# Kernel optimization log

Hardware: AMD Instinct MI355X
Metric: run time of the kernel (lower is better)

## Reference

```python
import jax, jax.numpy as jnp
import numpy as np

EMBED_DIM = 768
NUM_HEADS = 12
HEAD_DIM = EMBED_DIM // NUM_HEADS


def setup_inputs() -> dict:
    key = jax.random.key(0)
    ks = jax.random.split(key, 5)
    B, N, D = 8, 1024, EMBED_DIM
    s = 1.0 / np.sqrt(D)
    x = jax.random.normal(ks[0], (B, N, D), dtype=jnp.float32)
    W_qkv = jax.random.normal(ks[1], (D, 3 * D), dtype=jnp.float32) * s
    b_qkv = jnp.zeros((3 * D,), dtype=jnp.float32)
    W_proj = jax.random.normal(ks[2], (D, D), dtype=jnp.float32) * s
    b_proj = jnp.zeros((D,), dtype=jnp.float32)
    return {"x": x, "W_qkv": W_qkv, "b_qkv": b_qkv, "W_proj": W_proj, "b_proj": b_proj}


def reference(x, W_qkv, b_qkv, W_proj, b_proj):
    B, N, D = x.shape
    H, Hd = NUM_HEADS, HEAD_DIM
    scale = Hd ** -0.5
    qkv = x @ W_qkv + b_qkv                      # (B, N, 3D)
    qkv = qkv.reshape(B, N, 3, H, Hd).transpose(2, 0, 3, 1, 4)  # (3, B, H, N, Hd)
    q, k, v = qkv[0], qkv[1], qkv[2]
    attn = jnp.einsum('bhnd,bhmd->bhnm', q, k) * scale  # (B, H, N, N)
    attn = jax.nn.softmax(attn, axis=-1)
    out = jnp.einsum('bhnm,bhmd->bhnd', attn, v)        # (B, H, N, Hd)
    out = out.transpose(0, 2, 1, 3).reshape(B, N, D)
    return out @ W_proj + b_proj
```

## Files before the change

kernel.cpp:

```cpp
#include <hip/hip_runtime.h>


#define B_   8
#define N_   1024
#define D_   768
#define H_   12
#define HD_  64

typedef __attribute__((ext_vector_type(4))) float f32x4;
typedef __attribute__((ext_vector_type(8))) short bf16x8;

__device__ __forceinline__ unsigned short f2bf(float f) {
    unsigned int u = __float_as_uint(f);
    u += 0x7fff + ((u >> 16) & 1);
    return (unsigned short)(u >> 16);
}
__device__ __forceinline__ unsigned int pk2(float a, float b) {
    return (unsigned int)f2bf(a) | ((unsigned int)f2bf(b) << 16);
}
__device__ __forceinline__ unsigned int pk2t(float a, float b) {
    return __builtin_amdgcn_perm(__float_as_uint(b), __float_as_uint(a), 0x07060302u);
}
__device__ __forceinline__ float truncbf(float f) {
    return __uint_as_float(__float_as_uint(f) & 0xFFFF0000u);
}
__device__ __forceinline__ void gl_lds16(const void* g, void* l) {
    __builtin_amdgcn_global_load_lds(
        (const __attribute__((address_space(1))) unsigned int*)g,
        (__attribute__((address_space(3))) unsigned int*)l, 16, 0, 0);
}
#define MFMA(a, b, c) __builtin_amdgcn_mfma_f32_16x16x32_bf16(a, b, c, 0, 0, 0)
#define BAR() do { __asm__ volatile("" ::: "memory"); \
    __builtin_amdgcn_s_barrier(); \
    __asm__ volatile("" ::: "memory"); } while (0)
#define WAITVM(n) do { __asm__ volatile("" ::: "memory"); \
    __builtin_amdgcn_s_waitcnt(0xF70 | (n)); \
    __asm__ volatile("" ::: "memory"); } while (0)

__global__ __launch_bounds__(256) void prep_kernel(
    const float* __restrict__ x, const float* __restrict__ wqkv,
    const float* __restrict__ wproj,
    unsigned short* __restrict__ XB, unsigned short* __restrict__ WQT,
    unsigned short* __restrict__ WPT)
{
    const int bid = blockIdx.x;
    const int tid = threadIdx.x;
    if (bid < 3072) {
        int id = bid * 256 + tid;
        int r  = id & 127;
        int kc = (id >> 7) & 7;
        int ks = (id >> 10) % 12;
        int nt = id / 12288;
        const float* src = x + (size_t)(nt * 128 + r) * 768 + ks * 64 + kc * 8;
        float4 f0 = *(const float4*)src;
        float4 f1 = *(const float4*)(src + 4);
        uint4 o;
        o.x = pk2(f0.x, f0.y); o.y = pk2(f0.z, f0.w);
        o.z = pk2(f1.x, f1.y); o.w = pk2(f1.z, f1.w);
        *(uint4*)&XB[(size_t)id * 8] = o;
    } else if (bid < 3936) {
        int id = (bid - 3072) * 256 + tid;
        int fr = id & 127;
        int kc = (id >> 7) & 7;
        int ks = (id >> 10) % 12;
        int mt = id / 12288;
        float v[8];
#pragma unroll
        for (int j = 0; j < 8; ++j)
            v[j] = wqkv[(size_t)(ks * 64 + kc * 8 + j) * 2304 + mt * 128 + fr];
        uint4 o;
        o.x = pk2(v[0], v[1]); o.y = pk2(v[2], v[3]);
        o.z = pk2(v[4], v[5]); o.w = pk2(v[6], v[7]);
        *(uint4*)&WQT[(size_t)id * 8] = o;
    } else {
        int id = (bid - 3936) * 256 + tid;
        int fr = id & 63;
        int kc = (id >> 6) & 7;
        int ks = (id >> 9) % 12;
        int nt = id / 6144;
        float v[8];
#pragma unroll
        for (int j = 0; j < 8; ++j)
            v[j] = wproj[(size_t)(ks * 64 + kc * 8 + j) * 768 + nt * 64 + fr];
        uint4 o;
        o.x = pk2(v[0], v[1]); o.y = pk2(v[2], v[3]);
        o.z = pk2(v[4], v[5]); o.w = pk2(v[6], v[7]);
        *(uint4*)&WPT[(size_t)id * 8] = o;
    }
}

__global__ __launch_bounds__(256, 4) void qkv_gemm(
    const unsigned short* __restrict__ XB,
    const unsigned short* __restrict__ WQT,
    const float* __restrict__ bias,
    unsigned short* __restrict__ QS,
    unsigned short* __restrict__ KS,
    unsigned short* __restrict__ VS)
{
    __shared__ __align__(16) unsigned short As[2][4096];
    __shared__ __align__(16) unsigned short Bs[2][4096];

    const int tid = threadIdx.x;
    const int w = tid >> 6, lane = tid & 63;
    const int l15 = lane & 15, quad = lane >> 4;
    const int mt = blockIdx.x >> 6;
    const int nt = blockIdx.x & 63;
    const int m0w = (w & 1) * 64, n0w = (w >> 1) * 64;

    const char* baseA = (const char*)(WQT + (size_t)(mt * 12) * 8192);
    const char* baseB = (const char*)(XB  + (size_t)(nt * 12) * 8192);

    auto issue = [&](int ks) {
        const char* sA = baseA + ks * 8192;
        const char* sB = baseB + ks * 8192;
        const int pb = ks & 1;
#pragma unroll
        for (int i = 0; i < 2; ++i) {
            const int c = w * 2 + i;
            gl_lds16(sA + (c * 64 + lane) * 16, (char*)As + pb * 8192 + c * 1024);
            gl_lds16(sB + (c * 64 + lane) * 16, (char*)Bs + pb * 8192 + c * 1024);
        }
    };

    f32x4 acc[4][4];
    const f32x4 z = {0.f, 0.f, 0.f, 0.f};
#pragma unroll
    for (int t = 0; t < 4; ++t)
#pragma unroll
        for (int u = 0; u < 4; ++u) acc[t][u] = z;

    issue(0);
    for (int ks = 0; ks < 24; ++ks) {
        BAR();
        if (ks < 23) { issue(ks + 1); WAITVM(4); } else { WAITVM(0); }
        BAR();
        const unsigned short* Ab = As[ks & 1];
        const unsigned short* Bb = Bs[ks & 1];
        bf16x8 af[4], bfv[4];
#pragma unroll
        for (int t = 0; t < 4; ++t)
            af[t] = *(const bf16x8*)(Ab + (quad * 128 + m0w + t * 16 + l15) * 8);
#pragma unroll
        for (int u = 0; u < 4; ++u)
            bfv[u] = *(const bf16x8*)(Bb + (quad * 128 + n0w + u * 16 + l15) * 8);
#pragma unroll
        for (int t = 0; t < 4; ++t)
#pragma unroll
            for (int u = 0; u < 4; ++u)
                acc[t][u] = MFMA(af[t], bfv[u], acc[t][u]);
    }

    const int part = mt / 6;
#pragma unroll
    for (int t = 0; t < 4; ++t) {
        int flocal = (mt % 6) * 128 + m0w + t * 16 + quad * 4;
        float4 bv = *(const float4*)&bias[part * 768 + flocal];
        int h = flocal >> 6, d0 = flocal & 63;
#pragma unroll
        for (int u = 0; u < 4; ++u) {
            int token = nt * 128 + n0w + u * 16 + l15;
            int b = token >> 10, n = token & 1023;
            int bh = b * H_ + h;
            f32x4 a = acc[t][u];
            float v0 = a[0] + bv.x, v1 = a[1] + bv.y;
            float v2 = a[2] + bv.z, v3 = a[3] + bv.w;
            if (part == 0) {
                int qt = n >> 7, r = n & 127;
                size_t idx = ((size_t)(bh * 8 + qt) * 1024 + (d0 >> 3) * 128 + r) * 8 + (d0 & 7);
                uint2 pp; pp.x = pk2(v0, v1); pp.y = pk2(v2, v3);
                *(uint2*)&QS[idx] = pp;
            } else if (part == 1) {
                int kt = n >> 6, r = n & 63;
                size_t idx = ((size_t)(bh * 16 + kt) * 512 + (d0 >> 3) * 64 + r) * 8 + (d0 & 7);
                uint2 pp; pp.x = pk2(v0, v1); pp.y = pk2(v2, v3);
                *(uint2*)&KS[idx] = pp;
            } else {
                int kt = n >> 6, r = n & 63;
                size_t base = ((size_t)(bh * 16 + kt) * 512 + (r >> 3) * 64 + d0) * 8 + (r & 7);
                VS[base]      = f2bf(v0);
                VS[base + 8]  = f2bf(v1);
                VS[base + 16] = f2bf(v2);
                VS[base + 24] = f2bf(v3);
            }
        }
    }
}

__global__ __launch_bounds__(256, 3) void attn_kernel(
    const unsigned short* __restrict__ QS,
    const unsigned short* __restrict__ KS,
    const unsigned short* __restrict__ VS,
    unsigned short* __restrict__ AWS)
{
    __shared__ __align__(16) unsigned short Qs[8192];
    __shared__ __align__(16) unsigned short Ks[2][4096];
    __shared__ __align__(16) unsigned short Vs[2][4096];

    const int tid = threadIdx.x;
    const int w = tid >> 6, lane = tid & 63;
    const int l15 = lane & 15, quad = lane >> 4;
    const int bh = blockIdx.x % 96;
    const int qt = blockIdx.x / 96;
    const float C = 0.18033688f;

    const char* kbase = (const char*)(KS + (size_t)(bh * 16) * 4096);
    const char* vbase = (const char*)(VS + (size_t)(bh * 16) * 4096);

    auto issue_tile = [&](int kt) {
        const char* ks_ = kbase + kt * 8192;
        const char* vs_ = vbase + kt * 8192;
        const int pb = kt & 1;
#pragma unroll
        for (int i = 0; i < 2; ++i) {
            const int c = w * 2 + i;
            gl_lds16(ks_ + (c * 64 + lane) * 16, (char*)Ks + pb * 8192 + c * 1024);
            gl_lds16(vs_ + (c * 64 + lane) * 16, (char*)Vs + pb * 8192 + c * 1024);
        }
    };

    const char* qslab = (const char*)(QS + (size_t)(bh * 8 + qt) * 8192);
#pragma unroll
    for (int i = 0; i < 4; ++i) {
        const int c = w * 4 + i;
        gl_lds16(qslab + (c * 64 + lane) * 16, (char*)Qs + c * 1024);
    }
    issue_tile(0);

    WAITVM(4);
    BAR();
    bf16x8 qf[2][2];
#pragma unroll
    for (int u = 0; u < 2; ++u)
#pragma unroll
        for (int s = 0; s < 2; ++s)
            qf[u][s] = *(const bf16x8*)(Qs + ((s * 4 + quad) * 128 + w * 32 + u * 16 + l15) * 8);

    f32x4 o[4][2];
    const f32x4 z = {0.f, 0.f, 0.f, 0.f};
#pragma unroll
    for (int t = 0; t < 4; ++t) { o[t][0] = z; o[t][1] = z; }
    float lsum[2] = {0.f, 0.f};

    for (int kt = 0; kt < 16; ++kt) {
        BAR();
        if (kt < 15) { issue_tile(kt + 1); WAITVM(4); } else { WAITVM(0); }
        BAR();
        const unsigned short* Kb = Ks[kt & 1];
        const unsigned short* Vb = Vs[kt & 1];

        f32x4 s[4][2];
#pragma unroll
        for (int t = 0; t < 4; ++t) { s[t][0] = z; s[t][1] = z; }
#pragma unroll
        for (int ss = 0; ss < 2; ++ss) {
            bf16x8 kf[4];
#pragma unroll
            for (int t = 0; t < 4; ++t)
                kf[t] = *(const bf16x8*)(Kb + ((ss * 4 + quad) * 64 + t * 16 + l15) * 8);
#pragma unroll
            for (int t = 0; t < 4; ++t)
#pragma unroll
                for (int u = 0; u < 2; ++u)
                    s[t][u] = MFMA(kf[t], qf[u][ss], s[t][u]);
        }

        unsigned int pkk[2][4][2];
#pragma unroll
        for (int u = 0; u < 2; ++u) {
#pragma unroll
            for (int t = 0; t < 4; ++t) {
                float p0 = truncbf(__builtin_amdgcn_exp2f(s[t][u][0] * C));
                float p1 = truncbf(__builtin_amdgcn_exp2f(s[t][u][1] * C));
                float p2 = truncbf(__builtin_amdgcn_exp2f(s[t][u][2] * C));
                float p3 = truncbf(__builtin_amdgcn_exp2f(s[t][u][3] * C));
                lsum[u] += (p0 + p1) + (p2 + p3);
                pkk[u][t][0] = pk2t(p0, p1);
                pkk[u][t][1] = pk2t(p2, p3);
            }
        }

#pragma unroll
        for (int ss = 0; ss < 2; ++ss) {
            unsigned int bfr[2][4];
#pragma unroll
            for (int u = 0; u < 2; ++u)
#pragma unroll
                for (int jj = 0; jj < 4; ++jj) {
                    int sq = (quad & 1) * 2 + (jj >> 1);
                    int src = l15 + sq * 16;
                    int v0 = __shfl((int)pkk[u][2 * ss][jj & 1], src, 64);
                    int v1 = __shfl((int)pkk[u][2 * ss + 1][jj & 1], src, 64);
                    bfr[u][jj] = (quad >> 1) ? (unsigned int)v1 : (unsigned int)v0;
                }
            bf16x8 vf[4];
#pragma unroll
            for (int t = 0; t < 4; ++t)
                vf[t] = *(const bf16x8*)(Vb + ((ss * 4 + quad) * 64 + t * 16 + l15) * 8);
#pragma unroll
            for (int u = 0; u < 2; ++u) {
                union { unsigned int uu[4]; bf16x8 v; } cv;
                cv.uu[0] = bfr[u][0]; cv.uu[1] = bfr[u][1];
                cv.uu[2] = bfr[u][2]; cv.uu[3] = bfr[u][3];
#pragma unroll
                for (int t = 0; t < 4; ++t)
                    o[t][u] = MFMA(vf[t], cv.v, o[t][u]);
            }
        }
    }

    float inv[2];
#pragma unroll
    for (int u = 0; u < 2; ++u) {
        float l = lsum[u];
        l += __shfl_xor(l, 16, 64);
        l += __shfl_xor(l, 32, 64);
        inv[u] = 1.f / l;
    }
    const int b = bh / H_, h = bh % H_;
    const int mt = b * 8 + qt;
#pragma unroll
    for (int t = 0; t < 4; ++t) {
        int d0 = t * 16 + quad * 4;
#pragma unroll
        for (int u = 0; u < 2; ++u) {
            int ql = w * 32 + u * 16 + l15;
            size_t idx = ((size_t)(mt * 12 + h) * 1024 + (d0 >> 3) * 128 + ql) * 8 + (d0 & 7);
            uint2 pp;
            pp.x = pk2(o[t][u][0] * inv[u], o[t][u][1] * inv[u]);
            pp.y = pk2(o[t][u][2] * inv[u], o[t][u][3] * inv[u]);
            *(uint2*)&AWS[idx] = pp;
        }
    }
}

__global__ __launch_bounds__(256, 3) void proj_gemm(
    const unsigned short* __restrict__ AWS,
    const unsigned short* __restrict__ WPT,
    const float* __restrict__ bias, float* __restrict__ out)
{
    __shared__ __align__(16) unsigned short As[2][8192];
    __shared__ __align__(16) unsigned short Bs[2][4096];

    const int tid = threadIdx.x;
    const int w = tid >> 6, lane = tid & 63;
    const int l15 = lane & 15, quad = lane >> 4;
    const int mt = blockIdx.x / 12;
    const int nt = blockIdx.x % 12;
    const int m0w = (w & 1) * 64, n0w = (w >> 1) * 32;

    const char* baseA = (const char*)(AWS + (size_t)(mt * 12) * 8192);
    const char* baseB = (const char*)(WPT + (size_t)(nt * 12) * 4096);

    auto issue = [&](int ks) {
        const char* sA = baseA + ks * 16384;
        const char* sB = baseB + ks * 8192;
        const int pb = ks & 1;
#pragma unroll
        for (int i = 0; i < 4; ++i) {
            const int c = w * 4 + i;
            gl_lds16(sA + (c * 64 + lane) * 16, (char*)As + pb * 16384 + c * 1024);
        }
#pragma unroll
        for (int i = 0; i < 2; ++i) {
            const int c = w * 2 + i;
            gl_lds16(sB + (c * 64 + lane) * 16, (char*)Bs + pb * 8192 + c * 1024);
        }
    };

    f32x4 acc[4][2];
    const f32x4 z = {0.f, 0.f, 0.f, 0.f};
#pragma unroll
    for (int t = 0; t < 4; ++t) { acc[t][0] = z; acc[t][1] = z; }

    issue(0);
    for (int ks = 0; ks < 12; ++ks) {
        BAR();
        if (ks < 11) { issue(ks + 1); WAITVM(6); } else { WAITVM(0); }
        BAR();
        const unsigned short* Ab = As[ks & 1];
        const unsigned short* Bb = Bs[ks & 1];
#pragma unroll
        for (int kk = 0; kk < 2; ++kk) {
            bf16x8 af[4], bfv[2];
#pragma unroll
            for (int t = 0; t < 4; ++t)
                af[t] = *(const bf16x8*)(Ab + (((kk * 4 + quad) * 128) + m0w + t * 16 + l15) * 8);
#pragma unroll
            for (int u = 0; u < 2; ++u)
                bfv[u] = *(const bf16x8*)(Bb + (((kk * 4 + quad) * 64) + n0w + u * 16 + l15) * 8);
#pragma unroll
            for (int t = 0; t < 4; ++t)
#pragma unroll
                for (int u = 0; u < 2; ++u)
                    acc[t][u] = MFMA(af[t], bfv[u], acc[t][u]);
        }
    }

#pragma unroll
    for (int t = 0; t < 4; ++t)
#pragma unroll
        for (int u = 0; u < 2; ++u) {
            int col = nt * 64 + n0w + u * 16 + l15;
            float bvv = bias[col];
#pragma unroll
            for (int r = 0; r < 4; ++r) {
                int row = mt * 128 + m0w + t * 16 + quad * 4 + r;
                out[(size_t)row * 768 + col] = acc[t][u][r] + bvv;
            }
        }
}

extern "C" void kernel_launch(void* const* d_in, const int* in_sizes, int n_in,
                              void* d_out, int out_size, void* d_ws, size_t ws_size,
                              hipStream_t stream) {
    const float* x     = (const float*)d_in[0];
    const float* Wqkv  = (const float*)d_in[1];
    const float* bqkv  = (const float*)d_in[2];
    const float* Wproj = (const float*)d_in[3];
    const float* bproj = (const float*)d_in[4];
    float* out = (float*)d_out;

    unsigned short* ws = (unsigned short*)d_ws;
    unsigned short* XB  = ws;
    unsigned short* WQT = ws + 6291456;
    unsigned short* WPT = ws + 8060928;
    unsigned short* QS  = ws + 8650752;
    unsigned short* KS  = ws + 14942208;
    unsigned short* VS  = ws + 21233664;
    unsigned short* AWS = ws + 27525120;

    prep_kernel<<<dim3(4224), dim3(256), 0, stream>>>(x, Wqkv, Wproj, XB, WQT, WPT);
    qkv_gemm<<<dim3(18 * 64), dim3(256), 0, stream>>>(XB, WQT, bqkv, QS, KS, VS);
    attn_kernel<<<dim3(96 * 8), dim3(256), 0, stream>>>(QS, KS, VS, AWS);
    proj_gemm<<<dim3(64 * 12), dim3(256), 0, stream>>>(AWS, WPT, bproj, out);
}
```

Baseline: 194.2 us.

## Stage GEMM/attention epilogues through LDS and move P relayout from shuffles to LDS

The QKV GEMM epilogue now writes results into a swizzled LDS tile and then stores full 16-byte vectors to the Q/K/V tiled layouts, instead of scattered 8-byte and 2-byte global stores. The softmax scale is folded into Q at the GEMM epilogue, which removes a multiply per score in attention. In attention, the P-fragment relayout that used many cross-lane shuffles now goes through a per-wave swizzled LDS scratch area, and the output epilogue is also staged through LDS for coalesced 16-byte stores. The cost is extra barriers and LDS traffic, and the Q tile region is reused as scratch after Q fragments are loaded into registers.

```diff
diff --git a/kernel.cpp b/kernel.cpp
--- a/kernel.cpp
+++ b/kernel.cpp
@@ -36,6 +36,7 @@
 #define WAITVM(n) do { __asm__ volatile("" ::: "memory"); \
     __builtin_amdgcn_s_waitcnt(0xF70 | (n)); \
     __asm__ volatile("" ::: "memory"); } while (0)
+#define WAITLGKM() __asm__ volatile("s_waitcnt lgkmcnt(0)" ::: "memory")
 
 __global__ __launch_bounds__(256) void prep_kernel(
     const float* __restrict__ x, const float* __restrict__ wqkv,
@@ -97,8 +98,7 @@
     unsigned short* __restrict__ KS,
     unsigned short* __restrict__ VS)
 {
-    __shared__ __align__(16) unsigned short As[2][4096];
-    __shared__ __align__(16) unsigned short Bs[2][4096];
+    __shared__ __align__(16) unsigned short sm[16384];
 
     const int tid = threadIdx.x;
     const int w = tid >> 6, lane = tid & 63;
@@ -106,7 +106,9 @@
     const int mt = blockIdx.x >> 6;
     const int nt = blockIdx.x & 63;
     const int m0w = (w & 1) * 64, n0w = (w >> 1) * 64;
-
+    const float CS = 0.18033688f;
+
+    char* smb = (char*)sm;
     const char* baseA = (const char*)(WQT + (size_t)(mt * 12) * 8192);
     const char* baseB = (const char*)(XB  + (size_t)(nt * 12) * 8192);
 
@@ -117,8 +119,8 @@
 #pragma unroll
         for (int i = 0; i < 2; ++i) {
             const int c = w * 2 + i;
-            gl_lds16(sA + (c * 64 + lane) * 16, (char*)As + pb * 8192 + c * 1024);
-            gl_lds16(sB + (c * 64 + lane) * 16, (char*)Bs + pb * 8192 + c * 1024);
+            gl_lds16(sA + (c * 64 + lane) * 16, smb + pb * 8192 + c * 1024);
+            gl_lds16(sB + (c * 64 + lane) * 16, smb + 16384 + pb * 8192 + c * 1024);
         }
     };
 
@@ -134,8 +136,8 @@
         BAR();
         if (ks < 23) { issue(ks + 1); WAITVM(4); } else { WAITVM(0); }
         BAR();
-        const unsigned short* Ab = As[ks & 1];
-        const unsigned short* Bb = Bs[ks & 1];
+        const unsigned short* Ab = sm + (ks & 1) * 4096;
+        const unsigned short* Bb = sm + 8192 + (ks & 1) * 4096;
         bf16x8 af[4], bfv[4];
 #pragma unroll
         for (int t = 0; t < 4; ++t)
@@ -151,37 +153,71 @@
     }
 
     const int part = mt / 6;
+    BAR();
+
 #pragma unroll
     for (int t = 0; t < 4; ++t) {
-        int flocal = (mt % 6) * 128 + m0w + t * 16 + quad * 4;
-        float4 bv = *(const float4*)&bias[part * 768 + flocal];
-        int h = flocal >> 6, d0 = flocal & 63;
+        int d = m0w + t * 16 + quad * 4;
+        float4 bv = *(const float4*)&bias[part * 768 + (mt % 6) * 128 + d];
 #pragma unroll
         for (int u = 0; u < 4; ++u) {
-            int token = nt * 128 + n0w + u * 16 + l15;
-            int b = token >> 10, n = token & 1023;
-            int bh = b * H_ + h;
+            int tok = n0w + u * 16 + l15;
             f32x4 a = acc[t][u];
             float v0 = a[0] + bv.x, v1 = a[1] + bv.y;
             float v2 = a[2] + bv.z, v3 = a[3] + bv.w;
-            if (part == 0) {
-                int qt = n >> 7, r = n & 127;
-                size_t idx = ((size_t)(bh * 8 + qt) * 1024 + (d0 >> 3) * 128 + r) * 8 + (d0 & 7);
+            if (part == 0) { v0 *= CS; v1 *= CS; v2 *= CS; v3 *= CS; }
+            if (part < 2) {
+                unsigned off = tok * 256 + (((unsigned)(d * 2)) ^ ((tok & 7) << 4));
                 uint2 pp; pp.x = pk2(v0, v1); pp.y = pk2(v2, v3);
-                *(uint2*)&QS[idx] = pp;
-            } else if (part == 1) {
-                int kt = n >> 6, r = n & 63;
-                size_t idx = ((size_t)(bh * 16 + kt) * 512 + (d0 >> 3) * 64 + r) * 8 + (d0 & 7);
-                uint2 pp; pp.x = pk2(v0, v1); pp.y = pk2(v2, v3);
-                *(uint2*)&KS[idx] = pp;
+                *(uint2*)(smb + off) = pp;
             } else {
-                int kt = n >> 6, r = n & 63;
-                size_t base = ((size_t)(bh * 16 + kt) * 512 + (r >> 3) * 64 + d0) * 8 + (r & 7);
-                VS[base]      = f2bf(v0);
-                VS[base + 8]  = f2bf(v1);
-                VS[base + 16] = f2bf(v2);
-                VS[base + 24] = f2bf(v3);
+                float vv[4] = {v0, v1, v2, v3};
+#pragma unroll
+                for (int r4 = 0; r4 < 4; ++r4) {
+                    int dd = d + r4;
+                    unsigned off = dd * 256 + (((unsigned)(tok * 2)) ^ ((dd & 7) << 4));
+                    *(unsigned short*)(smb + off) = f2bf(vv[r4]);
+                }
             }
+        }
+    }
+    BAR();
+
+    const int b = nt >> 3, qtc = nt & 7;
+    if (part == 0) {
+#pragma unroll
+        for (int round = 0; round < 8; ++round) {
+            int r = tid & 127;
+            int kc = (tid >> 7) + round * 2;
+            uint4 val = *(const uint4*)(smb + r * 256 +
+                        (((unsigned)(kc << 4)) ^ ((r & 7) << 4)));
+            int h = (mt % 6) * 2 + (kc >> 3);
+            int bh = b * H_ + h;
+            *(uint4*)(QS + (((size_t)(bh * 8 + qtc) * 1024) + (kc & 7) * 128 + r) * 8) = val;
+        }
+    } else if (part == 1) {
+#pragma unroll
+        for (int round = 0; round < 8; ++round) {
+            int r = tid & 127;
+            int kc = (tid >> 7) + round * 2;
+            uint4 val = *(const uint4*)(smb + r * 256 +
+                        (((unsigned)(kc << 4)) ^ ((r & 7) << 4)));
+            int h = (mt % 6) * 2 + (kc >> 3);
+            int bh = b * H_ + h;
+            int kt = (qtc << 1) | (r >> 6);
+            *(uint4*)(KS + (((size_t)(bh * 16 + kt) * 512) + (kc & 7) * 64 + (r & 63)) * 8) = val;
+        }
+    } else {
+#pragma unroll
+        for (int round = 0; round < 8; ++round) {
+            int dd = tid & 127;
+            int tc = (tid >> 7) + round * 2;
+            uint4 val = *(const uint4*)(smb + dd * 256 +
+                        (((unsigned)(tc << 4)) ^ ((dd & 7) << 4)));
+            int h = (mt % 6) * 2 + (dd >> 6);
+            int bh = b * H_ + h;
+            int kt = (qtc << 1) | (tc >> 3);
+            *(uint4*)(VS + (((size_t)(bh * 16 + kt) * 512) + (tc & 7) * 64 + (dd & 63)) * 8) = val;
         }
     }
 }
@@ -192,17 +228,15 @@
     const unsigned short* __restrict__ VS,
     unsigned short* __restrict__ AWS)
 {
-    __shared__ __align__(16) unsigned short Qs[8192];
-    __shared__ __align__(16) unsigned short Ks[2][4096];
-    __shared__ __align__(16) unsigned short Vs[2][4096];
+    __shared__ __align__(16) unsigned short sm[24576];
 
     const int tid = threadIdx.x;
     const int w = tid >> 6, lane = tid & 63;
     const int l15 = lane & 15, quad = lane >> 4;
     const int bh = blockIdx.x % 96;
     const int qt = blockIdx.x / 96;
-    const float C = 0.18033688f;
-
+
+    char* smb = (char*)sm;
     const char* kbase = (const char*)(KS + (size_t)(bh * 16) * 4096);
     const char* vbase = (const char*)(VS + (size_t)(bh * 16) * 4096);
 
@@ -213,8 +247,8 @@
 #pragma unroll
         for (int i = 0; i < 2; ++i) {
             const int c = w * 2 + i;
-            gl_lds16(ks_ + (c * 64 + lane) * 16, (char*)Ks + pb * 8192 + c * 1024);
-            gl_lds16(vs_ + (c * 64 + lane) * 16, (char*)Vs + pb * 8192 + c * 1024);
+            gl_lds16(ks_ + (c * 64 + lane) * 16, smb + 16384 + pb * 8192 + c * 1024);
+            gl_lds16(vs_ + (c * 64 + lane) * 16, smb + 32768 + pb * 8192 + c * 1024);
         }
     };
 
@@ -222,7 +256,7 @@
 #pragma unroll
     for (int i = 0; i < 4; ++i) {
         const int c = w * 4 + i;
-        gl_lds16(qslab + (c * 64 + lane) * 16, (char*)Qs + c * 1024);
+        gl_lds16(qslab + (c * 64 + lane) * 16, smb + c * 1024);
     }
     issue_tile(0);
 
@@ -233,7 +267,9 @@
     for (int u = 0; u < 2; ++u)
 #pragma unroll
         for (int s = 0; s < 2; ++s)
-            qf[u][s] = *(const bf16x8*)(Qs + ((s * 4 + quad) * 128 + w * 32 + u * 16 + l15) * 8);
+            qf[u][s] = *(const bf16x8*)(sm + ((s * 4 + quad) * 128 + w * 32 + u * 16 + l15) * 8);
+    WAITLGKM();
+    BAR();
 
     f32x4 o[4][2];
     const f32x4 z = {0.f, 0.f, 0.f, 0.f};
@@ -241,12 +277,14 @@
     for (int t = 0; t < 4; ++t) { o[t][0] = z; o[t][1] = z; }
     float lsum[2] = {0.f, 0.f};
 
+    char* pscr = smb + w * 4096;
+
     for (int kt = 0; kt < 16; ++kt) {
         BAR();
         if (kt < 15) { issue_tile(kt + 1); WAITVM(4); } else { WAITVM(0); }
         BAR();
-        const unsigned short* Kb = Ks[kt & 1];
-        const unsigned short* Vb = Vs[kt & 1];
+        const unsigned short* Kb = sm + 8192 + (kt & 1) * 4096;
+        const unsigned short* Vb = sm + 16384 + (kt & 1) * 4096;
 
         f32x4 s[4][2];
 #pragma unroll
@@ -264,46 +302,35 @@
                     s[t][u] = MFMA(kf[t], qf[u][ss], s[t][u]);
         }
 
-        unsigned int pkk[2][4][2];
 #pragma unroll
         for (int u = 0; u < 2; ++u) {
 #pragma unroll
             for (int t = 0; t < 4; ++t) {
-                float p0 = truncbf(__builtin_amdgcn_exp2f(s[t][u][0] * C));
-                float p1 = truncbf(__builtin_amdgcn_exp2f(s[t][u][1] * C));
-                float p2 = truncbf(__builtin_amdgcn_exp2f(s[t][u][2] * C));
-                float p3 = truncbf(__builtin_amdgcn_exp2f(s[t][u][3] * C));
+                float p0 = truncbf(__builtin_amdgcn_exp2f(s[t][u][0]));
+                float p1 = truncbf(__builtin_amdgcn_exp2f(s[t][u][1]));
+                float p2 = truncbf(__builtin_amdgcn_exp2f(s[t][u][2]));
+                float p3 = truncbf(__builtin_amdgcn_exp2f(s[t][u][3]));
                 lsum[u] += (p0 + p1) + (p2 + p3);
-                pkk[u][t][0] = pk2t(p0, p1);
-                pkk[u][t][1] = pk2t(p2, p3);
+                uint2 pw; pw.x = pk2t(p0, p1); pw.y = pk2t(p2, p3);
+                *(uint2*)(pscr + u * 2048 + l15 * 128 +
+                          ((t ^ (l15 & 3)) << 5) + quad * 8) = pw;
             }
         }
+        WAITLGKM();
 
 #pragma unroll
         for (int ss = 0; ss < 2; ++ss) {
-            unsigned int bfr[2][4];
-#pragma unroll
-            for (int u = 0; u < 2; ++u)
-#pragma unroll
-                for (int jj = 0; jj < 4; ++jj) {
-                    int sq = (quad & 1) * 2 + (jj >> 1);
-                    int src = l15 + sq * 16;
-                    int v0 = __shfl((int)pkk[u][2 * ss][jj & 1], src, 64);
-                    int v1 = __shfl((int)pkk[u][2 * ss + 1][jj & 1], src, 64);
-                    bfr[u][jj] = (quad >> 1) ? (unsigned int)v1 : (unsigned int)v0;
-                }
             bf16x8 vf[4];
 #pragma unroll
             for (int t = 0; t < 4; ++t)
                 vf[t] = *(const bf16x8*)(Vb + ((ss * 4 + quad) * 64 + t * 16 + l15) * 8);
 #pragma unroll
             for (int u = 0; u < 2; ++u) {
-                union { unsigned int uu[4]; bf16x8 v; } cv;
-                cv.uu[0] = bfr[u][0]; cv.uu[1] = bfr[u][1];
-                cv.uu[2] = bfr[u][2]; cv.uu[3] = bfr[u][3];
+                bf16x8 pf = *(const bf16x8*)(pscr + u * 2048 + l15 * 128 +
+                            (((2 * ss + (quad >> 1)) ^ (l15 & 3)) << 5) + (quad & 1) * 16);
 #pragma unroll
                 for (int t = 0; t < 4; ++t)
-                    o[t][u] = MFMA(vf[t], cv.v, o[t][u]);
+                    o[t][u] = MFMA(vf[t], pf, o[t][u]);
             }
         }
     }
@@ -316,20 +343,32 @@
         l += __shfl_xor(l, 32, 64);
         inv[u] = 1.f / l;
     }
-    const int b = bh / H_, h = bh % H_;
-    const int mt = b * 8 + qt;
+
+    BAR();
+    char* tb = smb + 16384;
 #pragma unroll
     for (int t = 0; t < 4; ++t) {
-        int d0 = t * 16 + quad * 4;
+        int d = t * 16 + quad * 4;
 #pragma unroll
         for (int u = 0; u < 2; ++u) {
-            int ql = w * 32 + u * 16 + l15;
-            size_t idx = ((size_t)(mt * 12 + h) * 1024 + (d0 >> 3) * 128 + ql) * 8 + (d0 & 7);
+            int q = w * 32 + u * 16 + l15;
             uint2 pp;
             pp.x = pk2(o[t][u][0] * inv[u], o[t][u][1] * inv[u]);
             pp.y = pk2(o[t][u][2] * inv[u], o[t][u][3] * inv[u]);
-            *(uint2*)&AWS[idx] = pp;
-        }
+            unsigned off = q * 128 + (((unsigned)(d * 2)) ^ ((q & 7) << 4));
+            *(uint2*)(tb + off) = pp;
+        }
+    }
+    BAR();
+    const int b = bh / H_, h = bh % H_;
+    const int mtA = b * 8 + qt;
+#pragma unroll
+    for (int round = 0; round < 4; ++round) {
+        int q = tid & 127;
+        int dc = (tid >> 7) + round * 2;
+        uint4 val = *(const uint4*)(tb + q * 128 +
+                    (((unsigned)(dc << 4)) ^ ((q & 7) << 4)));
+        *(uint4*)(AWS + (((size_t)(mtA * 12 + h) * 1024) + dc * 128 + q) * 8) = val;
     }
 }
 
```

New measurement: 192.9 us. Within noise of the previous version (-0.7%).
